# Kernel optimization log

Hardware: AMD Instinct MI355X
Metric: run time of the kernel (lower is better)

## Reference

```python
import jax, jax.numpy as jnp
import numpy as np

NUM_CLASSES = 10  # CINIC-10


def setup_inputs() -> dict:
    key = jax.random.key(0)
    k1, k2 = jax.random.split(key)
    embeddings = jax.random.normal(k1, (131072, 512), dtype=jnp.float32)
    labels = jax.random.randint(k2, (131072,), 0, NUM_CLASSES)
    return {"embeddings": embeddings, "labels": labels}


def reference(embeddings, labels):
    # Per-class mean (prototypes) as a segment reduction. With all classes
    # present, torch.unique(labels) == [0..9] sorted, so the remapped
    # target_indices equal labels directly.
    n = embeddings.shape[0]
    sums = jax.ops.segment_sum(embeddings, labels, num_segments=NUM_CLASSES)  # [C, d]
    counts = jax.ops.segment_sum(jnp.ones((n,), embeddings.dtype), labels,
                                 num_segments=NUM_CLASSES)                    # [C]
    prototypes = sums / counts[:, None]

    # Squared Euclidean distances: ||e||^2 + ||p||^2 - 2 e.p  (== cdist(...)**2)
    sq_e = jnp.sum(embeddings * embeddings, axis=1, keepdims=True)  # [B, 1]
    sq_p = jnp.sum(prototypes * prototypes, axis=1)                 # [C]
    d2 = sq_e + sq_p[None, :] - 2.0 * (embeddings @ prototypes.T)   # [B, C]
    d2 = jnp.maximum(d2, 0.0)

    logits = -d2
    logp = jax.nn.log_softmax(logits, axis=-1)
    loss = -jnp.mean(jnp.take_along_axis(logp, labels[:, None], axis=1))
    return (loss, logits)
```

## Files before the change

### kernel.cpp

```cpp
#include <hip/hip_runtime.h>

#define NROWS   131072
#define DIMS    512
#define NC      10
#define SEG_BLOCKS 1024
#define SUMSTRIDE 5120

typedef __attribute__((ext_vector_type(8))) short short8;
typedef __attribute__((ext_vector_type(4))) float floatx4;


static __device__ __forceinline__ unsigned int pk2(float lo, float hi) {
    return (__float_as_uint(hi) & 0xFFFF0000u) | (__float_as_uint(lo) >> 16);
}

static __device__ __forceinline__ short8 pack8(const float4 a, const float4 b) {
    union { unsigned int u[4]; short8 v; } r;
    r.u[0] = pk2(a.x, a.y);
    r.u[1] = pk2(a.z, a.w);
    r.u[2] = pk2(b.x, b.y);
    r.u[3] = pk2(b.z, b.w);
    return r.v;
}


__global__ __launch_bounds__(256) void k_seg(const float* __restrict__ E,
                                             const int* __restrict__ L,
                                             float* __restrict__ part,
                                             int* __restrict__ counts) {
    __shared__ float4 R[NC * 128];
    __shared__ int lc[16];
    const int tid  = threadIdx.x;
    const int half = tid >> 7;
    const int dt   = tid & 127;
    if (tid < 16) lc[tid] = 0;
    __syncthreads();

    const int rows0 = blockIdx.x * 128;
    const float4* Ev = (const float4*)E;

    float4 z = {0.f, 0.f, 0.f, 0.f};
    float4 a0=z,a1=z,a2=z,a3=z,a4=z,a5=z,a6=z,a7=z,a8=z,a9=z;

    int idx = (rows0 + half) * 128 + dt;
    float4 v0 = Ev[idx];
    float4 v1 = Ev[idx + 256];
    int l0 = L[rows0 + half];
    int l1 = L[rows0 + 2 + half];

    for (int i = 0; i < 64; ++i) {
        float4 v2; int l2;
        const bool pf = (i < 62);
        if (pf) {
            v2 = Ev[idx + 512];
            l2 = L[rows0 + 2 * i + 4 + half];
        }
        if (dt == 0) atomicAdd(&lc[l0], 1);
        switch (l0) {
            case 0: a0.x+=v0.x; a0.y+=v0.y; a0.z+=v0.z; a0.w+=v0.w; break;
            case 1: a1.x+=v0.x; a1.y+=v0.y; a1.z+=v0.z; a1.w+=v0.w; break;
            case 2: a2.x+=v0.x; a2.y+=v0.y; a2.z+=v0.z; a2.w+=v0.w; break;
            case 3: a3.x+=v0.x; a3.y+=v0.y; a3.z+=v0.z; a3.w+=v0.w; break;
            case 4: a4.x+=v0.x; a4.y+=v0.y; a4.z+=v0.z; a4.w+=v0.w; break;
            case 5: a5.x+=v0.x; a5.y+=v0.y; a5.z+=v0.z; a5.w+=v0.w; break;
            case 6: a6.x+=v0.x; a6.y+=v0.y; a6.z+=v0.z; a6.w+=v0.w; break;
            case 7: a7.x+=v0.x; a7.y+=v0.y; a7.z+=v0.z; a7.w+=v0.w; break;
            case 8: a8.x+=v0.x; a8.y+=v0.y; a8.z+=v0.z; a8.w+=v0.w; break;
            default: a9.x+=v0.x; a9.y+=v0.y; a9.z+=v0.z; a9.w+=v0.w; break;
        }
        v0 = v1; l0 = l1;
        if (pf) { v1 = v2; l1 = l2; }
        idx += 256;
    }

    if (half) {
        R[0*128+dt]=a0; R[1*128+dt]=a1; R[2*128+dt]=a2; R[3*128+dt]=a3;
        R[4*128+dt]=a4; R[5*128+dt]=a5; R[6*128+dt]=a6; R[7*128+dt]=a7;
        R[8*128+dt]=a8; R[9*128+dt]=a9;
    }
    __syncthreads();
    if (!half) {
        float4* dst = (float4*)(part + (size_t)blockIdx.x * SUMSTRIDE);
        float4 t;
#define MERGE_ST(c, ac)                                                       \
        t = R[(c)*128 + dt];                                                  \
        t.x += ac.x; t.y += ac.y; t.z += ac.z; t.w += ac.w;                   \
        dst[(c)*128 + dt] = t;
        MERGE_ST(0,a0) MERGE_ST(1,a1) MERGE_ST(2,a2) MERGE_ST(3,a3)
        MERGE_ST(4,a4) MERGE_ST(5,a5) MERGE_ST(6,a6) MERGE_ST(7,a7)
        MERGE_ST(8,a8) MERGE_ST(9,a9)
#undef MERGE_ST
    }
    if (tid < 16) counts[blockIdx.x * 16 + tid] = lc[tid];
}


__global__ __launch_bounds__(256) void k_red(const float* __restrict__ part,
                                             float* __restrict__ psum8) {
    __shared__ float m[128];
    const int t   = threadIdx.x;
    const int col = t & 127, kh = t >> 7;
    const int cc  = blockIdx.x % 40;
    const int kc  = blockIdx.x / 40;
    const int e   = cc * 128 + col;

    const float* base = part + (size_t)(kc * 128 + kh * 64) * SUMSTRIDE + e;
    float s0=0.f, s1=0.f, s2=0.f, s3=0.f;
    for (int j = 0; j < 64; j += 4) {
        s0 += base[(size_t)(j + 0) * SUMSTRIDE];
        s1 += base[(size_t)(j + 1) * SUMSTRIDE];
        s2 += base[(size_t)(j + 2) * SUMSTRIDE];
        s3 += base[(size_t)(j + 3) * SUMSTRIDE];
    }
    float s = (s0 + s1) + (s2 + s3);
    if (kh) m[col] = s;
    __syncthreads();
    if (!kh) psum8[kc * SUMSTRIDE + e] = s + m[col];
}


__global__ __launch_bounds__(512) void k_pp(const float* __restrict__ psum8,
                                            const int* __restrict__ counts,
                                            float* __restrict__ p2,
                                            float* __restrict__ pn,
                                            float* __restrict__ out) {
    __shared__ float P[16 * DIMS];
    __shared__ int tmp[512];
    __shared__ int cnt[16];
    const int t = threadIdx.x;

    {
        const int c0 = t & 15, chunk = t >> 4;
        int s = 0;
        for (int j = 0; j < 32; ++j) s += counts[(chunk * 32 + j) * 16 + c0];
        tmp[t] = s;
    }
    __syncthreads();
    if (t < 16) {
        int n = 0;
        for (int ch = 0; ch < 32; ++ch) n += tmp[ch * 16 + t];
        cnt[t] = n;
    }
    if (t == 0) out[0] = 0.f;
    __syncthreads();

    for (int e = t; e < 16 * DIMS; e += 512) {
        const int c = e >> 9;
        float val = 0.f;
        if (c < NC) {
            float s = 0.f;
#pragma unroll
            for (int j = 0; j < 8; ++j) s += psum8[j * SUMSTRIDE + e];
            val = 2.f * s / (float)cnt[c];
        }
        p2[e] = val;
        P[e] = val;
    }
    __syncthreads();

    const int w = t >> 6, lane = t & 63;
    const float4* Pv = (const float4*)P;
    for (int sdx = 0; sdx < 2; ++sdx) {
        const int c = w + sdx * 8;
        float4 a = Pv[c * 128 + lane * 2];
        float4 b = Pv[c * 128 + lane * 2 + 1];
        float ss = a.x*a.x + a.y*a.y + a.z*a.z + a.w*a.w
                 + b.x*b.x + b.y*b.y + b.z*b.z + b.w*b.w;
        ss += __shfl_xor(ss, 1);  ss += __shfl_xor(ss, 2);
        ss += __shfl_xor(ss, 4);  ss += __shfl_xor(ss, 8);
        ss += __shfl_xor(ss, 16); ss += __shfl_xor(ss, 32);
        if (lane == 0) pn[c] = 0.25f * ss;
    }
}


__global__ __launch_bounds__(256, 2) void k_main(const float* __restrict__ E,
                                                 const int* __restrict__ L,
                                                 const float* __restrict__ p2,
                                                 const float* __restrict__ pn,
                                                 float* __restrict__ out) {
    const int tid  = threadIdx.x;
    const int wid  = tid >> 6, lane = tid & 63;
    const int c16  = lane & 15, quad = lane >> 4;

    short8 bf[16];
    const float4* P = (const float4*)p2;
#pragma unroll
    for (int kt = 0; kt < 16; ++kt) {
        float4 a = P[c16 * 128 + kt * 8 + quad * 2];
        float4 b = P[c16 * 128 + kt * 8 + quad * 2 + 1];
        bf[kt] = pack8(a, b);
    }
    const float pnc = pn[c16];

    float lossp = 0.f;
    const int gw = blockIdx.x * 4 + wid;
    for (int t = gw; t < 8192; t += 4096) {
        const int tile  = 8191 - t;
        const int rbase = tile * 16;
        const float4* A = (const float4*)(E + (size_t)(rbase + c16) * DIMS);

        floatx4 acc = {0.f, 0.f, 0.f, 0.f};
        float nrm = 0.f;
#pragma unroll
        for (int kt = 0; kt < 16; ++kt) {
            float4 a = A[kt * 8 + quad * 2];
            float4 b = A[kt * 8 + quad * 2 + 1];
            nrm += a.x*a.x + a.y*a.y + a.z*a.z + a.w*a.w;
            nrm += b.x*b.x + b.y*b.y + b.z*b.z + b.w*b.w;
            acc = __builtin_amdgcn_mfma_f32_16x16x32_bf16(pack8(a, b), bf[kt],
                                                          acc, 0, 0, 0);
        }
        nrm += __shfl_xor(nrm, 16);
        nrm += __shfl_xor(nrm, 32);

#pragma unroll
        for (int i = 0; i < 4; ++i) {
            const int row = rbase + quad * 4 + i;
            const float nr = __shfl(nrm, quad * 4 + i);
            float lg = acc[i] - nr - pnc;
            lg = fminf(lg, 0.f);
            float ml = (c16 < NC) ? lg : -3.0e38f;
            ml = fmaxf(ml, __shfl_xor(ml, 1));
            ml = fmaxf(ml, __shfl_xor(ml, 2));
            ml = fmaxf(ml, __shfl_xor(ml, 4));
            ml = fmaxf(ml, __shfl_xor(ml, 8));
            float ex = (c16 < NC) ? __expf(lg - ml) : 0.f;
            ex += __shfl_xor(ex, 1);
            ex += __shfl_xor(ex, 2);
            ex += __shfl_xor(ex, 4);
            ex += __shfl_xor(ex, 8);
            const float lse = ml + __logf(ex);
            if (c16 < NC) out[1 + row * NC + c16] = lg;
            const int lab = L[row];
            if (c16 == lab) lossp += lse - lg;
        }
    }

    lossp += __shfl_xor(lossp, 1);  lossp += __shfl_xor(lossp, 2);
    lossp += __shfl_xor(lossp, 4);  lossp += __shfl_xor(lossp, 8);
    lossp += __shfl_xor(lossp, 16); lossp += __shfl_xor(lossp, 32);
    __shared__ float ls[4];
    if (lane == 0) ls[wid] = lossp;
    __syncthreads();
    if (tid == 0)
        atomicAdd(out, (ls[0] + ls[1] + ls[2] + ls[3]) * (1.0f / (float)NROWS));
}


extern "C" void kernel_launch(void* const* d_in, const int* in_sizes, int n_in,
                              void* d_out, int out_size, void* d_ws, size_t ws_size,
                              hipStream_t stream) {
    const float* E = (const float*)d_in[0];
    const int*   L = (const int*)d_in[1];
    float* out = (float*)d_out;
    char* ws = (char*)d_ws;

    float* part   = (float*)ws;
    float* psum8  = (float*)(ws + 20971520);
    int*   counts = (int*)  (ws + 21135360);
    float* p2     = (float*)(ws + 21200896);
    float* pn     = (float*)(ws + 21233664);

    k_seg <<<SEG_BLOCKS, 256, 0, stream>>>(E, L, part, counts);
    k_red <<<320,        256, 0, stream>>>(part, psum8);
    k_pp  <<<1,          512, 0, stream>>>(psum8, counts, p2, pn, out);
    k_main<<<1024,       256, 0, stream>>>(E, L, p2, pn, out);
}
```

Measured before the change: 453.3 us.

## Deepen k_seg load pipeline, stage labels in LDS, one tile per wave in k_main

The segment-sum kernel now stages the block's 128 labels in shared memory and counts them once up front. It then processes rows in double-buffered groups of four float4 loads, so more memory requests are in flight per thread and occupancy is hinted at 4 blocks. The main kernel drops its two-iteration tile loop, launches twice as many blocks with one tile per wave, and raises the launch-bounds occupancy hint to 3. The aim is more memory-level parallelism on this bandwidth-bound pass over the embeddings, at the cost of higher register pressure from the extra live loads.

```diff
diff --git a/kernel.cpp b/kernel.cpp
--- a/kernel.cpp
+++ b/kernel.cpp
@@ -24,54 +24,59 @@
 }
 
 
-__global__ __launch_bounds__(256) void k_seg(const float* __restrict__ E,
-                                             const int* __restrict__ L,
-                                             float* __restrict__ part,
-                                             int* __restrict__ counts) {
+__global__ __launch_bounds__(256, 4) void k_seg(const float* __restrict__ E,
+                                                const int* __restrict__ L,
+                                                float* __restrict__ part,
+                                                int* __restrict__ counts) {
     __shared__ float4 R[NC * 128];
+    __shared__ int lls[128];
     __shared__ int lc[16];
     const int tid  = threadIdx.x;
     const int half = tid >> 7;
     const int dt   = tid & 127;
+    const int rows0 = blockIdx.x * 128;
     if (tid < 16) lc[tid] = 0;
-    __syncthreads();
-
-    const int rows0 = blockIdx.x * 128;
-    const float4* Ev = (const float4*)E;
+    if (tid < 128) lls[tid] = L[rows0 + tid];
+    __syncthreads();
+    if (tid < 128) atomicAdd(&lc[lls[tid]], 1);
+
+    const float4* Ev = (const float4*)E + (size_t)(rows0 + half) * 128 + dt;
 
     float4 z = {0.f, 0.f, 0.f, 0.f};
     float4 a0=z,a1=z,a2=z,a3=z,a4=z,a5=z,a6=z,a7=z,a8=z,a9=z;
 
-    int idx = (rows0 + half) * 128 + dt;
-    float4 v0 = Ev[idx];
-    float4 v1 = Ev[idx + 256];
-    int l0 = L[rows0 + half];
-    int l1 = L[rows0 + 2 + half];
-
-    for (int i = 0; i < 64; ++i) {
-        float4 v2; int l2;
-        const bool pf = (i < 62);
-        if (pf) {
-            v2 = Ev[idx + 512];
-            l2 = L[rows0 + 2 * i + 4 + half];
-        }
-        if (dt == 0) atomicAdd(&lc[l0], 1);
-        switch (l0) {
-            case 0: a0.x+=v0.x; a0.y+=v0.y; a0.z+=v0.z; a0.w+=v0.w; break;
-            case 1: a1.x+=v0.x; a1.y+=v0.y; a1.z+=v0.z; a1.w+=v0.w; break;
-            case 2: a2.x+=v0.x; a2.y+=v0.y; a2.z+=v0.z; a2.w+=v0.w; break;
-            case 3: a3.x+=v0.x; a3.y+=v0.y; a3.z+=v0.z; a3.w+=v0.w; break;
-            case 4: a4.x+=v0.x; a4.y+=v0.y; a4.z+=v0.z; a4.w+=v0.w; break;
-            case 5: a5.x+=v0.x; a5.y+=v0.y; a5.z+=v0.z; a5.w+=v0.w; break;
-            case 6: a6.x+=v0.x; a6.y+=v0.y; a6.z+=v0.z; a6.w+=v0.w; break;
-            case 7: a7.x+=v0.x; a7.y+=v0.y; a7.z+=v0.z; a7.w+=v0.w; break;
-            case 8: a8.x+=v0.x; a8.y+=v0.y; a8.z+=v0.z; a8.w+=v0.w; break;
-            default: a9.x+=v0.x; a9.y+=v0.y; a9.z+=v0.z; a9.w+=v0.w; break;
-        }
-        v0 = v1; l0 = l1;
-        if (pf) { v1 = v2; l1 = l2; }
-        idx += 256;
-    }
+    float4 vA0,vA1,vA2,vA3, vB0,vB1,vB2,vB3;
+    int    lA0,lA1,lA2,lA3, lB0,lB1,lB2,lB3;
+
+#define LOADX(S, b)                                                           \
+    v##S##0 = Ev[(b)*1024 +   0];  v##S##1 = Ev[(b)*1024 + 256];              \
+    v##S##2 = Ev[(b)*1024 + 512];  v##S##3 = Ev[(b)*1024 + 768];              \
+    l##S##0 = lls[(b)*8 + half];       l##S##1 = lls[(b)*8 + 2 + half];       \
+    l##S##2 = lls[(b)*8 + 4 + half];   l##S##3 = lls[(b)*8 + 6 + half];
+
+#define ACC(v, l)                                                             \
+    switch (l) {                                                              \
+        case 0: a0.x+=v.x; a0.y+=v.y; a0.z+=v.z; a0.w+=v.w; break;            \
+        case 1: a1.x+=v.x; a1.y+=v.y; a1.z+=v.z; a1.w+=v.w; break;            \
+        case 2: a2.x+=v.x; a2.y+=v.y; a2.z+=v.z; a2.w+=v.w; break;            \
+        case 3: a3.x+=v.x; a3.y+=v.y; a3.z+=v.z; a3.w+=v.w; break;            \
+        case 4: a4.x+=v.x; a4.y+=v.y; a4.z+=v.z; a4.w+=v.w; break;            \
+        case 5: a5.x+=v.x; a5.y+=v.y; a5.z+=v.z; a5.w+=v.w; break;            \
+        case 6: a6.x+=v.x; a6.y+=v.y; a6.z+=v.z; a6.w+=v.w; break;            \
+        case 7: a7.x+=v.x; a7.y+=v.y; a7.z+=v.z; a7.w+=v.w; break;            \
+        case 8: a8.x+=v.x; a8.y+=v.y; a8.z+=v.z; a8.w+=v.w; break;            \
+        default: a9.x+=v.x; a9.y+=v.y; a9.z+=v.z; a9.w+=v.w; break;           \
+    }
+
+    LOADX(A, 0)
+    for (int p = 0; p < 8; ++p) {
+        LOADX(B, 2 * p + 1)
+        ACC(vA0, lA0) ACC(vA1, lA1) ACC(vA2, lA2) ACC(vA3, lA3)
+        if (p < 7) { LOADX(A, 2 * p + 2) }
+        ACC(vB0, lB0) ACC(vB1, lB1) ACC(vB2, lB2) ACC(vB3, lB3)
+    }
+#undef LOADX
+#undef ACC
 
     if (half) {
         R[0*128+dt]=a0; R[1*128+dt]=a1; R[2*128+dt]=a2; R[3*128+dt]=a3;
@@ -174,7 +179,7 @@
 }
 
 
-__global__ __launch_bounds__(256, 2) void k_main(const float* __restrict__ E,
+__global__ __launch_bounds__(256, 3) void k_main(const float* __restrict__ E,
                                                  const int* __restrict__ L,
                                                  const float* __restrict__ p2,
                                                  const float* __restrict__ pn,
@@ -193,48 +198,45 @@
     }
     const float pnc = pn[c16];
 
+    const int tile  = 8191 - (blockIdx.x * 4 + wid);
+    const int rbase = tile * 16;
+    const float4* A = (const float4*)(E + (size_t)(rbase + c16) * DIMS);
+
+    floatx4 acc = {0.f, 0.f, 0.f, 0.f};
+    float nrm = 0.f;
+#pragma unroll
+    for (int kt = 0; kt < 16; ++kt) {
+        float4 a = A[kt * 8 + quad * 2];
+        float4 b = A[kt * 8 + quad * 2 + 1];
+        nrm += a.x*a.x + a.y*a.y + a.z*a.z + a.w*a.w;
+        nrm += b.x*b.x + b.y*b.y + b.z*b.z + b.w*b.w;
+        acc = __builtin_amdgcn_mfma_f32_16x16x32_bf16(pack8(a, b), bf[kt],
+                                                      acc, 0, 0, 0);
+    }
+    nrm += __shfl_xor(nrm, 16);
+    nrm += __shfl_xor(nrm, 32);
+
     float lossp = 0.f;
-    const int gw = blockIdx.x * 4 + wid;
-    for (int t = gw; t < 8192; t += 4096) {
-        const int tile  = 8191 - t;
-        const int rbase = tile * 16;
-        const float4* A = (const float4*)(E + (size_t)(rbase + c16) * DIMS);
-
-        floatx4 acc = {0.f, 0.f, 0.f, 0.f};
-        float nrm = 0.f;
-#pragma unroll
-        for (int kt = 0; kt < 16; ++kt) {
-            float4 a = A[kt * 8 + quad * 2];
-            float4 b = A[kt * 8 + quad * 2 + 1];
-            nrm += a.x*a.x + a.y*a.y + a.z*a.z + a.w*a.w;
-            nrm += b.x*b.x + b.y*b.y + b.z*b.z + b.w*b.w;
-            acc = __builtin_amdgcn_mfma_f32_16x16x32_bf16(pack8(a, b), bf[kt],
-                                                          acc, 0, 0, 0);
-        }
-        nrm += __shfl_xor(nrm, 16);
-        nrm += __shfl_xor(nrm, 32);
-
-#pragma unroll
-        for (int i = 0; i < 4; ++i) {
-            const int row = rbase + quad * 4 + i;
-            const float nr = __shfl(nrm, quad * 4 + i);
-            float lg = acc[i] - nr - pnc;
-            lg = fminf(lg, 0.f);
-            float ml = (c16 < NC) ? lg : -3.0e38f;
-            ml = fmaxf(ml, __shfl_xor(ml, 1));
-            ml = fmaxf(ml, __shfl_xor(ml, 2));
-            ml = fmaxf(ml, __shfl_xor(ml, 4));
-            ml = fmaxf(ml, __shfl_xor(ml, 8));
-            float ex = (c16 < NC) ? __expf(lg - ml) : 0.f;
-            ex += __shfl_xor(ex, 1);
-            ex += __shfl_xor(ex, 2);
-            ex += __shfl_xor(ex, 4);
-            ex += __shfl_xor(ex, 8);
-            const float lse = ml + __logf(ex);
-            if (c16 < NC) out[1 + row * NC + c16] = lg;
-            const int lab = L[row];
-            if (c16 == lab) lossp += lse - lg;
-        }
+#pragma unroll
+    for (int i = 0; i < 4; ++i) {
+        const int row = rbase + quad * 4 + i;
+        const float nr = __shfl(nrm, quad * 4 + i);
+        float lg = acc[i] - nr - pnc;
+        lg = fminf(lg, 0.f);
+        float ml = (c16 < NC) ? lg : -3.0e38f;
+        ml = fmaxf(ml, __shfl_xor(ml, 1));
+        ml = fmaxf(ml, __shfl_xor(ml, 2));
+        ml = fmaxf(ml, __shfl_xor(ml, 4));
+        ml = fmaxf(ml, __shfl_xor(ml, 8));
+        float ex = (c16 < NC) ? __expf(lg - ml) : 0.f;
+        ex += __shfl_xor(ex, 1);
+        ex += __shfl_xor(ex, 2);
+        ex += __shfl_xor(ex, 4);
+        ex += __shfl_xor(ex, 8);
+        const float lse = ml + __logf(ex);
+        if (c16 < NC) out[1 + row * NC + c16] = lg;
+        const int lab = L[row];
+        if (c16 == lab) lossp += lse - lg;
     }
 
     lossp += __shfl_xor(lossp, 1);  lossp += __shfl_xor(lossp, 2);
@@ -265,5 +267,5 @@
     k_seg <<<SEG_BLOCKS, 256, 0, stream>>>(E, L, part, counts);
     k_red <<<320,        256, 0, stream>>>(part, psum8);
     k_pp  <<<1,          512, 0, stream>>>(psum8, counts, p2, pn, out);
-    k_main<<<1024,       256, 0, stream>>>(E, L, p2, pn, out);
-}
+    k_main<<<2048,       256, 0, stream>>>(E, L, p2, pn, out);
+}
```

New measurement: 456.8 us. About the same (+0.8%).
